# Kernel tuning notes

Hardware: AMD Instinct MI355X
Metric: run time of the kernel (lower is better)

The kernel has to match this reference:

```python
import jax, jax.numpy as jnp
import numpy as np

C = 256
B, H, W = 16, 64, 64
CQK = C // 8


def setup_inputs() -> dict:
    key = jax.random.key(0)
    ks = jax.random.split(key, 8)
    s = 0.02
    return {
        "x": jax.random.normal(ks[0], (B, C, H, W), dtype=jnp.float32),
        "Wq": jax.random.normal(ks[1], (CQK, C), dtype=jnp.float32) * s,
        "bq": jax.random.normal(ks[2], (CQK,), dtype=jnp.float32) * s,
        "Wk": jax.random.normal(ks[3], (CQK, C), dtype=jnp.float32) * s,
        "bk": jax.random.normal(ks[4], (CQK,), dtype=jnp.float32) * s,
        "Wv": jax.random.normal(ks[5], (C, C), dtype=jnp.float32) * s,
        "bv": jax.random.normal(ks[6], (C,), dtype=jnp.float32) * s,
        "gamma": jax.random.normal(ks[7], (1,), dtype=jnp.float32) * 0.1,
    }


def reference(x, Wq, bq, Wk, bk, Wv, bv, gamma):
    b, c, h, w = x.shape
    n = h * w
    xf = x.reshape(b, c, n)  # flatten spatial -> tokens
    # 1x1 convs are per-token linear maps over channels
    q = jnp.einsum('oc,bcn->bon', Wq, xf) + bq[None, :, None]  # [B, C/8, N]
    k = jnp.einsum('oc,bcn->bon', Wk, xf) + bk[None, :, None]  # [B, C/8, N]
    v = jnp.einsum('oc,bcn->bon', Wv, xf) + bv[None, :, None]  # [B, C,   N]
    attn = jnp.einsum('bdi,bdj->bij', q, k)        # [B, N, N] = Q^T K
    attn = jax.nn.softmax(attn, axis=2)            # softmax over keys
    out = jnp.einsum('bcj,bij->bci', v, attn)      # V @ attn^T -> [B, C, N]
    out = out.reshape(b, c, h, w)
    return gamma[0] * out + x
```

## Files before the change

kernel.cpp:

```cpp
#include <hip/hip_runtime.h>
#include <hip/hip_bf16.h>

#define BB   16
#define CCH  256
#define DQK  32
#define NTOK 4096

typedef __attribute__((ext_vector_type(8)))  short short8;
typedef __attribute__((ext_vector_type(4)))  float f32x4;
typedef __attribute__((ext_vector_type(16))) float f32x16;
typedef unsigned short u16t;
typedef unsigned int   u32t;
typedef long long      i64t;

__device__ __forceinline__ u16t f2bf(float f){
  u32t u = __builtin_bit_cast(u32t, f);
  u += 0x7FFFu + ((u >> 16) & 1u);
  return (u16t)(u >> 16);
}
__device__ __forceinline__ u32t pk2(float a, float b){
  return (u32t)f2bf(a) | ((u32t)f2bf(b) << 16);
}
__device__ __forceinline__ void lane32swap(u32t& a, u32t& b){
  asm("v_permlane32_swap_b32 %0, %1" : "+v"(a), "+v"(b));
}
__device__ __forceinline__ float swapadd(float x){
  u32t a = __builtin_bit_cast(u32t, x), b = a;
  lane32swap(a, b);
  return __builtin_bit_cast(float, a) + __builtin_bit_cast(float, b);
}
__device__ __forceinline__ void gload16(const void* g, void* l){
  __builtin_amdgcn_global_load_lds(
      (const __attribute__((address_space(1))) void*)g,
      (__attribute__((address_space(3))) void*)l, 16, 0, 0);
}
__device__ __forceinline__ f32x16 zero16(){
  f32x16 z;
  #pragma unroll
  for (int i = 0; i < 16; ++i) z[i] = 0.f;
  return z;
}
#define mfma32(A, B, C)  __builtin_amdgcn_mfma_f32_32x32x16_bf16((A), (B), (C), 0, 0, 0)
#define mfma8(A, B, C)   __builtin_amdgcn_mfma_f32_32x32x16_fp8_fp8((A), (B), (C), 0, 0, 0)
__device__ __forceinline__ u32t pack4fp8(float a, float b, float c, float d){
  int t = __builtin_amdgcn_cvt_pk_fp8_f32(a, b, 0, false);
  t = __builtin_amdgcn_cvt_pk_fp8_f32(c, d, t, true);
  return (u32t)t;
}
__device__ __forceinline__ unsigned char tofp8(float v){
  return (unsigned char)(__builtin_amdgcn_cvt_pk_fp8_f32(v, 0.f, 0, false) & 0xFF);
}

__global__ __launch_bounds__(256) void k_wconv(const float* __restrict__ Wq,
    const float* __restrict__ Wk, const float* __restrict__ Wv,
    u16t* __restrict__ o){
  const int base = (blockIdx.x * 256 + threadIdx.x) * 4;
  float4 v;
  if (base < 8192)        v = *(const float4*)(Wq + base);
  else if (base < 16384)  v = *(const float4*)(Wk + base - 8192);
  else                    v = *(const float4*)(Wv + base - 16384);
  *(uint2*)(o + base) = make_uint2(pk2(v.x, v.y), pk2(v.z, v.w));
}

__global__ __launch_bounds__(256) void k_proj(const float* __restrict__ x,
    const u16t* __restrict__ Wb,
    const float* __restrict__ bq, const float* __restrict__ bk,
    const float* __restrict__ bv,
    u16t* __restrict__ Q, u16t* __restrict__ K, unsigned char* __restrict__ V){
  __shared__ __align__(16) u16t xt[32 * 512];
  const int b = blockIdx.y, nb = blockIdx.x * 64;
  const int tid = threadIdx.x;
  const int w = tid >> 6, lane = tid & 63;
  const int lo = lane & 15, g = lane >> 4;

  const float* xb = x + (size_t)b * CCH * NTOK + nb;
  const int cg = tid >> 4, n0 = (tid & 15) * 4;
  #pragma unroll
  for (int rep = 0; rep < 16; ++rep){
    const int c = rep * 16 + cg;
    float4 v = *(const float4*)(xb + (size_t)c * NTOK + n0);
    const int chunkb = (n0 >> 4) * 8 + (c >> 5);
    const int fl = 16 * ((c >> 3) & 3);
    const int e = c & 7;
    xt[chunkb * 512 + ((n0 & 15) + 0 + fl) * 8 + e] = f2bf(v.x);
    xt[chunkb * 512 + ((n0 & 15) + 1 + fl) * 8 + e] = f2bf(v.y);
    xt[chunkb * 512 + ((n0 & 15) + 2 + fl) * 8 + e] = f2bf(v.z);
    xt[chunkb * 512 + ((n0 & 15) + 3 + fl) * 8 + e] = f2bf(v.w);
  }
  __syncthreads();

  #pragma unroll
  for (int ot = 0; ot < 5; ++ot){
    const u16t* Wrow; const float* bias; int ob; int mode;
    if (ot == 0){
      if (w < 2){ Wrow = Wb;        bias = bq; ob = w * 16;       mode = 0; }
      else      { Wrow = Wb + 8192; bias = bk; ob = (w - 2) * 16; mode = 1; }
    } else { Wrow = Wb + 16384; bias = bv; ob = (ot - 1) * 64 + w * 16; mode = 2; }
    const u16t* wp = Wrow + (size_t)(ob + lo) * CCH + g * 8;

    f32x4 acc[4];
    #pragma unroll
    for (int s = 0; s < 4; ++s) acc[s] = (f32x4){0.f, 0.f, 0.f, 0.f};
    #pragma unroll
    for (int kc = 0; kc < CCH; kc += 32){
      const short8 af = *(const short8*)(wp + kc);
      #pragma unroll
      for (int s = 0; s < 4; ++s){
        const short8 bf = *(const short8*)(xt + (s * 8 + (kc >> 5)) * 512 + lane * 8);
        acc[s] = __builtin_amdgcn_mfma_f32_16x16x32_bf16(af, bf, acc[s], 0, 0, 0);
      }
    }
    #pragma unroll
    for (int s = 0; s < 4; ++s){
      #pragma unroll
      for (int r = 0; r < 4; ++r){
        const int o = ob + 4 * g + r;
        const int n = nb + s * 16 + lo;
        float val = acc[s][r] + bias[o];
        if (mode == 0){
          val *= 1.44269504088896f;
          Q[((size_t)b * NTOK + n) * DQK + o] = f2bf(val);
        } else if (mode == 1){
          K[((size_t)b * NTOK + n) * DQK + o] = f2bf(val);
        } else {
          const int swz = ((((s * 2) + (lo >> 3)) ^ ((o >> 1) & 7)) << 3) + (lo & 7);
          V[((size_t)b * CCH + o) * (size_t)NTOK + nb + swz] = tofp8(val);
        }
      }
    }
  }
}

__global__ __launch_bounds__(256, 2) void k_attn(
    const u16t* __restrict__ Q, const u16t* __restrict__ K,
    const unsigned char* __restrict__ V,
    const float* __restrict__ x, const float* __restrict__ gamma,
    float* __restrict__ out){
  __shared__ __align__(16) u16t KT[2 * 2048];
  __shared__ __align__(16) unsigned char Vt[2][16384];
  const int bid = blockIdx.x;
  const int b  = ((bid & 7) << 1) | ((bid >> 3) & 1);
  const int qt = bid >> 4;
  const int tid = threadIdx.x, w = tid >> 6, lane = tid & 63;
  const int ql = lane & 31, hi = lane >> 5;
  const int qg = qt * 128 + w * 32;

  const u16t* Qb = Q + (size_t)b * NTOK * DQK;
  const u16t* Kb = K + (size_t)b * NTOK * DQK;
  const unsigned char* Vb = V + (size_t)b * CCH * NTOK;

  const short8 qf0 = *(const short8*)(Qb + (size_t)(qg + ql) * DQK + hi * 8);
  const short8 qf1 = *(const short8*)(Qb + (size_t)(qg + ql) * DQK + 16 + hi * 8);

  f32x16 acc[8];
  #pragma unroll
  for (int c = 0; c < 8; ++c) acc[c] = zero16();
  float l = 0.f;

  const char* vsrc0 = (const char*)Vb + (size_t)(w * 64 + (lane >> 2)) * NTOK + (lane & 3) * 16;
  const size_t kse = (size_t)((w & 1) * 32 + ql) * DQK + (w >> 1) * 16 + hi * 8;
  const char* ksrc0 = (const char*)Kb + kse * 2;
  const int kla = lane * 16;
  int vaddA[4], vaddB[4];
  #pragma unroll
  for (int kt = 0; kt < 4; ++kt){
    vaddA[kt] = ql * 64 + (((kt * 2 + hi) ^ ((ql >> 1) & 7)) << 3);
    vaddB[kt] = vaddA[kt] + 16384;
  }
  const char* ldsV = (const char*)&Vt[0][0];
  const char* ldsK = (const char*)&KT[0];
  u32t pf2[4][2];

  #define PACK_PF8(S0, S1) \
    { _Pragma("unroll") \
      for (int kt_ = 0; kt_ < 4; ++kt_){ \
        const int bo = (kt_ & 1) * 8; \
        u32t A, B; \
        if (kt_ < 2){ \
          A = pack4fp8(S0[bo+0], S0[bo+1], S0[bo+2], S0[bo+3]); \
          B = pack4fp8(S0[bo+4], S0[bo+5], S0[bo+6], S0[bo+7]); \
        } else { \
          A = pack4fp8(S1[bo+0], S1[bo+1], S1[bo+2], S1[bo+3]); \
          B = pack4fp8(S1[bo+4], S1[bo+5], S1[bo+6], S1[bo+7]); \
        } \
        lane32swap(A, B); \
        pf2[kt_][0] = A; pf2[kt_][1] = B; \
      } }

  #define QK_STEP(KRD, S0, S1) \
    { const char* kb_ = ldsK + (KRD) * 4096; \
      const short8 kf00 = *(const short8*)(kb_ + kla + 0 * 1024); \
      const short8 kf10 = *(const short8*)(kb_ + kla + 1 * 1024); \
      const short8 kf01 = *(const short8*)(kb_ + kla + 2 * 1024); \
      const short8 kf11 = *(const short8*)(kb_ + kla + 3 * 1024); \
      S0 = mfma32(kf00, qf0, zero16()); S0 = mfma32(kf01, qf1, S0); \
      S1 = mfma32(kf10, qf0, zero16()); S1 = mfma32(kf11, qf1, S1); }

  #define ESL(S, B) \
    { S[(B)+0] = __builtin_amdgcn_exp2f(S[(B)+0]); r0 += S[(B)+0]; \
      S[(B)+1] = __builtin_amdgcn_exp2f(S[(B)+1]); r1 += S[(B)+1]; \
      S[(B)+2] = __builtin_amdgcn_exp2f(S[(B)+2]); r2 += S[(B)+2]; \
      S[(B)+3] = __builtin_amdgcn_exp2f(S[(B)+3]); r3 += S[(B)+3]; }

  #define PVCHUNK(CS, VRD, EXPSLICE) \
    { const i64t vf0 = *(const i64t*)(ldsV + ((VRD)?vaddB[0]:vaddA[0]) + (CS)*2048); \
      const i64t vf1 = *(const i64t*)(ldsV + ((VRD)?vaddB[1]:vaddA[1]) + (CS)*2048); \
      const i64t vf2 = *(const i64t*)(ldsV + ((VRD)?vaddB[2]:vaddA[2]) + (CS)*2048); \
      const i64t vf3 = *(const i64t*)(ldsV + ((VRD)?vaddB[3]:vaddA[3]) + (CS)*2048); \
      acc[CS] = mfma8(vf0, pb0, acc[CS]); \
      acc[CS] = mfma8(vf1, pb1, acc[CS]); \
      acc[CS] = mfma8(vf2, pb2, acc[CS]); \
      acc[CS] = mfma8(vf3, pb3, acc[CS]); \
      EXPSLICE \
      __builtin_amdgcn_sched_group_barrier(0x100, 4, 0); \
      __builtin_amdgcn_sched_group_barrier(0x8,   4, 0); \
      __builtin_amdgcn_sched_group_barrier(0x2,  10, 0); }

  #define NOSL
  #define PBDEFS \
      const i64t pb0 = __builtin_bit_cast(i64t, make_uint2(pf2[0][0], pf2[0][1])); \
      const i64t pb1 = __builtin_bit_cast(i64t, make_uint2(pf2[1][0], pf2[1][1])); \
      const i64t pb2 = __builtin_bit_cast(i64t, make_uint2(pf2[2][0], pf2[2][1])); \
      const i64t pb3 = __builtin_bit_cast(i64t, make_uint2(pf2[3][0], pf2[3][1]));

  #define ABODY(T, VRD, KRD, KST) { \
      const int toff_ = ((T) + 1) * 64; \
      _Pragma("unroll") \
      for (int i = 0; i < 4; ++i) \
        gload16(vsrc0 + (size_t)i * 16 * NTOK + toff_, &Vt[(VRD)^1][w * 4096 + i * 1024]); \
      { const int kt2_ = ((T) + 2 <= 63) ? (T) + 2 : 63; \
        gload16(ksrc0 + (size_t)kt2_ * 4096, &KT[(KST) * 2048 + w * 512]); } \
      f32x16 s0, s1; \
      QK_STEP(KRD, s0, s1); \
      PBDEFS \
      float r0 = 0.f, r1 = 0.f, r2 = 0.f, r3 = 0.f; \
      PVCHUNK(0, VRD, ESL(s0, 0)) \
      PVCHUNK(1, VRD, ESL(s0, 4)) \
      PVCHUNK(2, VRD, ESL(s0, 8)) \
      PVCHUNK(3, VRD, ESL(s0, 12)) \
      PVCHUNK(4, VRD, ESL(s1, 0)) \
      PVCHUNK(5, VRD, ESL(s1, 4)) \
      PVCHUNK(6, VRD, ESL(s1, 8)) \
      PVCHUNK(7, VRD, ESL(s1, 12)) \
      l += (r0 + r1) + (r2 + r3); \
      PACK_PF8(s0, s1); \
      __syncthreads(); }

  #pragma unroll
  for (int i = 0; i < 4; ++i)
    gload16(vsrc0 + (size_t)i * 16 * NTOK, &Vt[0][w * 4096 + i * 1024]);
  gload16(ksrc0,        &KT[0 * 2048 + w * 512]);
  gload16(ksrc0 + 4096, &KT[1 * 2048 + w * 512]);
  __syncthreads();

  {
    f32x16 s0, s1;
    QK_STEP(0, s0, s1);
    float r0 = 0.f, r1 = 0.f, r2 = 0.f, r3 = 0.f;
    ESL(s0, 0) ESL(s0, 4) ESL(s0, 8) ESL(s0, 12)
    ESL(s1, 0) ESL(s1, 4) ESL(s1, 8) ESL(s1, 12)
    l = (r0 + r1) + (r2 + r3);
    PACK_PF8(s0, s1);
  }
  __syncthreads();

  for (int t = 0; t < 62; t += 2){
    ABODY(t,     0, 1, 0)
    ABODY(t + 1, 1, 0, 1)
  }
  ABODY(62, 0, 1, 0)

  {
    PBDEFS
    PVCHUNK(0, 1, NOSL) PVCHUNK(1, 1, NOSL) PVCHUNK(2, 1, NOSL) PVCHUNK(3, 1, NOSL)
    PVCHUNK(4, 1, NOSL) PVCHUNK(5, 1, NOSL) PVCHUNK(6, 1, NOSL) PVCHUNK(7, 1, NOSL)
  }

  const float lfull = swapadd(l);
  const float inv = 1.0f / lfull;
  const float gm = gamma[0];
  const int n = qg + ql;
  #pragma unroll
  for (int cs = 0; cs < 8; ++cs){
    #pragma unroll
    for (int r = 0; r < 16; ++r){
      const int c = cs * 32 + (r & 3) + 8 * (r >> 2) + 4 * hi;
      const size_t idx = ((size_t)b * CCH + c) * NTOK + n;
      out[idx] = gm * (acc[cs][r] * inv) + x[idx];
    }
  }
  #undef PACK_PF8
  #undef QK_STEP
  #undef ESL
  #undef PVCHUNK
  #undef NOSL
  #undef PBDEFS
  #undef ABODY
}

extern "C" void kernel_launch(void* const* d_in, const int* in_sizes, int n_in,
                              void* d_out, int out_size, void* d_ws, size_t ws_size,
                              hipStream_t stream) {
  const float* x     = (const float*)d_in[0];
  const float* Wq    = (const float*)d_in[1];
  const float* bq    = (const float*)d_in[2];
  const float* Wk    = (const float*)d_in[3];
  const float* bk    = (const float*)d_in[4];
  const float* Wv    = (const float*)d_in[5];
  const float* bv    = (const float*)d_in[6];
  const float* gamma = (const float*)d_in[7];
  float* out = (float*)d_out;

  char* ws = (char*)d_ws;
  u16t* Qw = (u16t*)(ws);
  u16t* Kw = (u16t*)(ws + 4194304);
  unsigned char* Vw = (unsigned char*)(ws + 8388608);
  u16t* Wbf = (u16t*)d_out;

  hipLaunchKernelGGL(k_wconv, dim3(80), dim3(256), 0, stream, Wq, Wk, Wv, Wbf);
  hipLaunchKernelGGL(k_proj, dim3(NTOK / 64, BB), dim3(256), 0, stream,
                     x, Wbf, bq, bk, bv, Qw, Kw, Vw);
  hipLaunchKernelGGL(k_attn, dim3(512), dim3(256), 0, stream,
                     Qw, Kw, Vw, x, gamma, out);
}
```

Baseline: 168.3 us.

## Split attention output channels across two wave groups with 512-thread blocks

Doubles the attention block to 8 waves. Each group of four query waves now owns half of the 256 output channels, so the per-wave accumulator shrinks from 8 to 4 f32x16 tiles and register pressure drops. The QK^T and exp work is duplicated across the two channel halves. K tile loads are limited to the first four waves, V loads are spread over all eight, and the schedule hints are retuned. The aim is more resident waves per CU to hide latency, at the cost of recomputing QK/softmax and larger blocks.

Result: slower. 199.9 us (+18.8%).

```diff
diff --git a/kernel.cpp b/kernel.cpp
--- a/kernel.cpp
+++ b/kernel.cpp
@@ -131,7 +131,7 @@
   }
 }
 
-__global__ __launch_bounds__(256, 2) void k_attn(
+__global__ __launch_bounds__(512, 4) void k_attn(
     const u16t* __restrict__ Q, const u16t* __restrict__ K,
     const unsigned char* __restrict__ V,
     const float* __restrict__ x, const float* __restrict__ gamma,
@@ -142,31 +142,30 @@
   const int b  = ((bid & 7) << 1) | ((bid >> 3) & 1);
   const int qt = bid >> 4;
   const int tid = threadIdx.x, w = tid >> 6, lane = tid & 63;
+  const int qg = w & 3, ch = w >> 2;
   const int ql = lane & 31, hi = lane >> 5;
-  const int qg = qt * 128 + w * 32;
+  const int qgb = qt * 128 + qg * 32;
 
   const u16t* Qb = Q + (size_t)b * NTOK * DQK;
   const u16t* Kb = K + (size_t)b * NTOK * DQK;
   const unsigned char* Vb = V + (size_t)b * CCH * NTOK;
 
-  const short8 qf0 = *(const short8*)(Qb + (size_t)(qg + ql) * DQK + hi * 8);
-  const short8 qf1 = *(const short8*)(Qb + (size_t)(qg + ql) * DQK + 16 + hi * 8);
-
-  f32x16 acc[8];
-  #pragma unroll
-  for (int c = 0; c < 8; ++c) acc[c] = zero16();
+  const short8 qf0 = *(const short8*)(Qb + (size_t)(qgb + ql) * DQK + hi * 8);
+  const short8 qf1 = *(const short8*)(Qb + (size_t)(qgb + ql) * DQK + 16 + hi * 8);
+
+  f32x16 acc[4];
+  #pragma unroll
+  for (int c = 0; c < 4; ++c) acc[c] = zero16();
   float l = 0.f;
 
-  const char* vsrc0 = (const char*)Vb + (size_t)(w * 64 + (lane >> 2)) * NTOK + (lane & 3) * 16;
+  const char* vsrc0 = (const char*)Vb + (size_t)(w * 32 + (lane >> 2)) * NTOK + (lane & 3) * 16;
   const size_t kse = (size_t)((w & 1) * 32 + ql) * DQK + (w >> 1) * 16 + hi * 8;
   const char* ksrc0 = (const char*)Kb + kse * 2;
   const int kla = lane * 16;
-  int vaddA[4], vaddB[4];
-  #pragma unroll
-  for (int kt = 0; kt < 4; ++kt){
-    vaddA[kt] = ql * 64 + (((kt * 2 + hi) ^ ((ql >> 1) & 7)) << 3);
-    vaddB[kt] = vaddA[kt] + 16384;
-  }
+  int vadd[4];
+  #pragma unroll
+  for (int kt = 0; kt < 4; ++kt)
+    vadd[kt] = (ch * 128 + ql) * 64 + (((kt * 2 + hi) ^ ((ql >> 1) & 7)) << 3);
   const char* ldsV = (const char*)&Vt[0][0];
   const char* ldsK = (const char*)&KT[0];
   u32t pf2[4][2];
@@ -203,10 +202,10 @@
       S[(B)+3] = __builtin_amdgcn_exp2f(S[(B)+3]); r3 += S[(B)+3]; }
 
   #define PVCHUNK(CS, VRD, EXPSLICE) \
-    { const i64t vf0 = *(const i64t*)(ldsV + ((VRD)?vaddB[0]:vaddA[0]) + (CS)*2048); \
-      const i64t vf1 = *(const i64t*)(ldsV + ((VRD)?vaddB[1]:vaddA[1]) + (CS)*2048); \
-      const i64t vf2 = *(const i64t*)(ldsV + ((VRD)?vaddB[2]:vaddA[2]) + (CS)*2048); \
-      const i64t vf3 = *(const i64t*)(ldsV + ((VRD)?vaddB[3]:vaddA[3]) + (CS)*2048); \
+    { const i64t vf0 = *(const i64t*)(ldsV + vadd[0] + (VRD)*16384 + (CS)*2048); \
+      const i64t vf1 = *(const i64t*)(ldsV + vadd[1] + (VRD)*16384 + (CS)*2048); \
+      const i64t vf2 = *(const i64t*)(ldsV + vadd[2] + (VRD)*16384 + (CS)*2048); \
+      const i64t vf3 = *(const i64t*)(ldsV + vadd[3] + (VRD)*16384 + (CS)*2048); \
       acc[CS] = mfma8(vf0, pb0, acc[CS]); \
       acc[CS] = mfma8(vf1, pb1, acc[CS]); \
       acc[CS] = mfma8(vf2, pb2, acc[CS]); \
@@ -214,7 +213,7 @@
       EXPSLICE \
       __builtin_amdgcn_sched_group_barrier(0x100, 4, 0); \
       __builtin_amdgcn_sched_group_barrier(0x8,   4, 0); \
-      __builtin_amdgcn_sched_group_barrier(0x2,  10, 0); }
+      __builtin_amdgcn_sched_group_barrier(0x2,  16, 0); }
 
   #define NOSL
   #define PBDEFS \
@@ -226,31 +225,29 @@
   #define ABODY(T, VRD, KRD, KST) { \
       const int toff_ = ((T) + 1) * 64; \
       _Pragma("unroll") \
-      for (int i = 0; i < 4; ++i) \
-        gload16(vsrc0 + (size_t)i * 16 * NTOK + toff_, &Vt[(VRD)^1][w * 4096 + i * 1024]); \
-      { const int kt2_ = ((T) + 2 <= 63) ? (T) + 2 : 63; \
+      for (int i = 0; i < 2; ++i) \
+        gload16(vsrc0 + (size_t)i * 16 * NTOK + toff_, &Vt[(VRD)^1][w * 2048 + i * 1024]); \
+      if (w < 4){ const int kt2_ = ((T) + 2 <= 63) ? (T) + 2 : 63; \
         gload16(ksrc0 + (size_t)kt2_ * 4096, &KT[(KST) * 2048 + w * 512]); } \
       f32x16 s0, s1; \
       QK_STEP(KRD, s0, s1); \
       PBDEFS \
       float r0 = 0.f, r1 = 0.f, r2 = 0.f, r3 = 0.f; \
-      PVCHUNK(0, VRD, ESL(s0, 0)) \
-      PVCHUNK(1, VRD, ESL(s0, 4)) \
-      PVCHUNK(2, VRD, ESL(s0, 8)) \
-      PVCHUNK(3, VRD, ESL(s0, 12)) \
-      PVCHUNK(4, VRD, ESL(s1, 0)) \
-      PVCHUNK(5, VRD, ESL(s1, 4)) \
-      PVCHUNK(6, VRD, ESL(s1, 8)) \
-      PVCHUNK(7, VRD, ESL(s1, 12)) \
+      PVCHUNK(0, VRD, ESL(s0, 0) ESL(s0, 4)) \
+      PVCHUNK(1, VRD, ESL(s0, 8) ESL(s0, 12)) \
+      PVCHUNK(2, VRD, ESL(s1, 0) ESL(s1, 4)) \
+      PVCHUNK(3, VRD, ESL(s1, 8) ESL(s1, 12)) \
       l += (r0 + r1) + (r2 + r3); \
       PACK_PF8(s0, s1); \
       __syncthreads(); }
 
   #pragma unroll
-  for (int i = 0; i < 4; ++i)
-    gload16(vsrc0 + (size_t)i * 16 * NTOK, &Vt[0][w * 4096 + i * 1024]);
-  gload16(ksrc0,        &KT[0 * 2048 + w * 512]);
-  gload16(ksrc0 + 4096, &KT[1 * 2048 + w * 512]);
+  for (int i = 0; i < 2; ++i)
+    gload16(vsrc0 + (size_t)i * 16 * NTOK, &Vt[0][w * 2048 + i * 1024]);
+  if (w < 4){
+    gload16(ksrc0,        &KT[0 * 2048 + w * 512]);
+    gload16(ksrc0 + 4096, &KT[1 * 2048 + w * 512]);
+  }
   __syncthreads();
 
   {
@@ -272,19 +269,19 @@
 
   {
     PBDEFS
-    PVCHUNK(0, 1, NOSL) PVCHUNK(1, 1, NOSL) PVCHUNK(2, 1, NOSL) PVCHUNK(3, 1, NOSL)
-    PVCHUNK(4, 1, NOSL) PVCHUNK(5, 1, NOSL) PVCHUNK(6, 1, NOSL) PVCHUNK(7, 1, NOSL)
+    PVCHUNK(0, 1, NOSL) PVCHUNK(1, 1, NOSL)
+    PVCHUNK(2, 1, NOSL) PVCHUNK(3, 1, NOSL)
   }
 
   const float lfull = swapadd(l);
   const float inv = 1.0f / lfull;
   const float gm = gamma[0];
-  const int n = qg + ql;
-  #pragma unroll
-  for (int cs = 0; cs < 8; ++cs){
+  const int n = qgb + ql;
+  #pragma unroll
+  for (int cs = 0; cs < 4; ++cs){
     #pragma unroll
     for (int r = 0; r < 16; ++r){
-      const int c = cs * 32 + (r & 3) + 8 * (r >> 2) + 4 * hi;
+      const int c = ch * 128 + cs * 32 + (r & 3) + 8 * (r >> 2) + 4 * hi;
       const size_t idx = ((size_t)b * CCH + c) * NTOK + n;
       out[idx] = gm * (acc[cs][r] * inv) + x[idx];
     }
@@ -320,6 +317,6 @@
   hipLaunchKernelGGL(k_wconv, dim3(80), dim3(256), 0, stream, Wq, Wk, Wv, Wbf);
   hipLaunchKernelGGL(k_proj, dim3(NTOK / 64, BB), dim3(256), 0, stream,
                      x, Wbf, bq, bk, bv, Qw, Kw, Vw);
-  hipLaunchKernelGGL(k_attn, dim3(512), dim3(256), 0, stream,
+  hipLaunchKernelGGL(k_attn, dim3(512), dim3(512), 0, stream,
                      Qw, Kw, Vw, x, gamma, out);
 }
```
